# Kernel optimization log

Measured on AMD Instinct MI355X. Metric: run time of the kernel, lower is better.

The kernel has to match this reference:

```python
import jax, jax.numpy as jnp
import numpy as np

NUM_HEADS = 16
HEAD_DIM = 128  # hidden_size=2048 // num_heads=16


def setup_inputs() -> dict:
    key = jax.random.key(0)
    k1, k2, k3, k4, k5 = jax.random.split(key, 5)
    B, S, H = 4, 4096, 2048
    scale_in = 1.0 / np.sqrt(H)
    return {
        "x": jax.random.normal(k1, (B, S, H), dtype=jnp.float32),
        "Wqkv": jax.random.normal(k2, (H, 3 * H), dtype=jnp.float32) * scale_in,
        "bqkv": jax.random.normal(k3, (3 * H,), dtype=jnp.float32) * 0.01,
        "Wproj": jax.random.normal(k4, (H, H), dtype=jnp.float32) * scale_in,
        "bproj": jax.random.normal(k5, (H,), dtype=jnp.float32) * 0.01,
    }


def reference(x, Wqkv, bqkv, Wproj, bproj):
    B, S, hidden = x.shape
    H, D = NUM_HEADS, HEAD_DIM
    qkv = x @ Wqkv + bqkv                       # (B, S, 3*hidden)
    qkv = qkv.reshape(B, S, 3, H, D)
    q, k, v = qkv[:, :, 0], qkv[:, :, 1], qkv[:, :, 2]  # each (B, S, H, D)
    # Faithful to source: matmul over last two dims -> scores are (B, S, H, H)
    # (head-to-head attention per position; the repo never moved heads to dim 1).
    scores = jnp.einsum("bshd,bstd->bsht", q, k) / jnp.sqrt(jnp.asarray(D, x.dtype))
    weights = jax.nn.softmax(scores, axis=-1)    # (B, S, H, H)
    context = jnp.einsum("bsht,bstd->bshd", weights, v)  # (B, S, H, D)
    # Faithful reproduction of context.transpose(1, 2).contiguous().view(B, S, hidden)
    context = context.transpose(0, 2, 1, 3).reshape(B, S, hidden)
    return context @ Wproj + bproj
```

## Files before the change

kernel.cpp:

```cpp
#include <hip/hip_runtime.h>

typedef unsigned short u16;
typedef __attribute__((ext_vector_type(8))) short short8;
typedef __attribute__((ext_vector_type(4))) float float4v;

__device__ __forceinline__ u16 f2b(float f) {
  union { float f; unsigned u; } v; v.f = f;
  unsigned r = v.u + 0x7fffu + ((v.u >> 16) & 1u);
  return (u16)(r >> 16);
}

#define AS1(p) ((const __attribute__((address_space(1))) void*)(p))
#define AS3(p) ((__attribute__((address_space(3))) void*)(p))
#define MFMA16(a, b, c) __builtin_amdgcn_mfma_f32_16x16x32_bf16(a, b, c, 0, 0, 0)

__global__ __launch_bounds__(256) void cvt_bf16_kernel(const float* __restrict__ in,
                                                       u16* __restrict__ out, long n) {
  long i = ((long)blockIdx.x * 256 + threadIdx.x) * 8;
  if (i + 8 > n) return;
  float4v a = *(const float4v*)(in + i);
  float4v b = *(const float4v*)(in + i + 4);
  short8 o;
  o[0] = (short)f2b(a[0]); o[1] = (short)f2b(a[1]);
  o[2] = (short)f2b(a[2]); o[3] = (short)f2b(a[3]);
  o[4] = (short)f2b(b[0]); o[5] = (short)f2b(b[1]);
  o[6] = (short)f2b(b[2]); o[7] = (short)f2b(b[3]);
  *(short8*)(out + i) = o;
}

__global__ __launch_bounds__(256) void transpose_cvt_kernel(const float* __restrict__ in,
                                                            u16* __restrict__ out,
                                                            int rows, int cols) {
  __shared__ float tile[32][33];
  int bx = blockIdx.x * 32;
  int by = blockIdx.y * 32;
  int tx = threadIdx.x & 31, ty = threadIdx.x >> 5;
  for (int r = ty; r < 32; r += 8)
    tile[r][tx] = in[(long)(by + r) * cols + bx + tx];
  __syncthreads();
  for (int r = ty; r < 32; r += 8)
    out[(long)(bx + r) * rows + by + tx] = f2b(tile[tx][r]);
}

__global__ __launch_bounds__(512, 2) void gemm256_bt_bias(const u16* __restrict__ A,
                                                          const u16* __restrict__ B,
                                                          const float* __restrict__ bias,
                                                          void* __restrict__ Cout,
                                                          int M, int N, int K, int out_bf16) {
  __shared__ __align__(16) u16 As[2][2][8192];
  __shared__ __align__(16) u16 Bs[2][2][8192];

  const int t = threadIdx.x;
  const int lane = t & 63;
  const int w = t >> 6;
  const int wm = w >> 2;
  const int wn = w & 3;
  const int lm = lane & 15;
  const int lq = lane >> 4;

  const int nwg = gridDim.x * gridDim.y;
  const int orig = blockIdx.y * gridDim.x + blockIdx.x;
  const int qq = nwg >> 3, rr = nwg & 7;
  const int xcd = orig & 7, loc = orig >> 3;
  const int wgid = (xcd < rr ? xcd * (qq + 1) : rr * (qq + 1) + (xcd - rr) * qq) + loc;
  const int bx = wgid % gridDim.x;
  const int by = wgid / gridDim.x;

  const long row0 = (long)by * 256;
  const long col0 = (long)bx * 256;

  const int phys0 = t * 8;
  const int log0 = phys0 ^ (((phys0 >> 6) & 7) << 3);
  const long r0s = log0 >> 6; const int c0s = log0 & 63;
  const long r1s = r0s + 64;  const int c1s = c0s;

  const u16* Ag0 = A + (row0 + r0s) * K + c0s;
  const u16* Ag1 = A + (row0 + r1s) * K + c1s;
  const u16* Bg0 = B + (col0 + r0s) * K + c0s;
  const u16* Bg1 = B + (col0 + r1s) * K + c1s;
  const long hstride = 128L * (long)K;

  const int sb  = lm * 64 + ((lq * 8) ^ ((lm & 7) << 3));
  const int sbx = sb ^ 32;

  float4v acc[8][4] = {};
  const int NT = K >> 6;

  auto stA = [&](int buf, int h, int kt) {
    u16* d = &As[buf][h][0] + t * 8;
    const long ko = (long)kt * 64 + (long)h * hstride;
    __builtin_amdgcn_global_load_lds(AS1(Ag0 + ko), AS3(d), 16, 0, 0);
    __builtin_amdgcn_global_load_lds(AS1(Ag1 + ko), AS3(d + 4096), 16, 0, 0);
  };
  auto stB = [&](int buf, int h, int kt) {
    u16* d = &Bs[buf][h][0] + t * 8;
    const long ko = (long)kt * 64 + (long)h * hstride;
    __builtin_amdgcn_global_load_lds(AS1(Bg0 + ko), AS3(d), 16, 0, 0);
    __builtin_amdgcn_global_load_lds(AS1(Bg1 + ko), AS3(d + 4096), 16, 0, 0);
  };

  auto ktile = [&](int buf, int u) {
    asm volatile("" ::: "memory");
    const u16* Abl = &As[buf][wm][0] + sb;
    const u16* Abh = &As[buf][wm][0] + sbx;
    const u16* Bbl = &Bs[buf][wn >> 1][0] + (wn & 1) * 4096 + sb;
    const u16* Bbh = &Bs[buf][wn >> 1][0] + (wn & 1) * 4096 + sbx;
    const int kn  = (u + 1 < NT) ? u + 1 : NT - 1;
    const int kb2 = (u + 2 < NT) ? u + 2 : NT - 1;

    short8 bfr[4][2];
#pragma unroll
    for (int n = 0; n < 4; n++) {
      bfr[n][0] = *(const short8*)(Bbl + n * 1024);
      bfr[n][1] = *(const short8*)(Bbh + n * 1024);
    }
    {
      short8 a00 = *(const short8*)(Abl + 0);
      short8 a01 = *(const short8*)(Abh + 0);
      short8 a10 = *(const short8*)(Abl + 1024);
      short8 a11 = *(const short8*)(Abh + 1024);
      stA(buf ^ 1, 0, kn);
      asm volatile("s_waitcnt lgkmcnt(8)" ::: "memory");
      __builtin_amdgcn_s_barrier();
      asm volatile("s_waitcnt lgkmcnt(0)" ::: "memory");
      __builtin_amdgcn_s_setprio(1);
#pragma unroll
      for (int n = 0; n < 4; n++) {
        acc[0][n] = MFMA16(a00, bfr[n][0], acc[0][n]);
        acc[0][n] = MFMA16(a01, bfr[n][1], acc[0][n]);
        acc[1][n] = MFMA16(a10, bfr[n][0], acc[1][n]);
        acc[1][n] = MFMA16(a11, bfr[n][1], acc[1][n]);
      }
      __builtin_amdgcn_s_setprio(0);
      __builtin_amdgcn_s_barrier();
    }
#pragma unroll
    for (int p = 1; p < 4; p++) {
      short8 a00 = *(const short8*)(Abl + (2 * p) * 1024);
      short8 a01 = *(const short8*)(Abh + (2 * p) * 1024);
      short8 a10 = *(const short8*)(Abl + (2 * p + 1) * 1024);
      short8 a11 = *(const short8*)(Abh + (2 * p + 1) * 1024);
      if (p == 1)      stA(buf ^ 1, 1, kn);
      else if (p == 2) stB(buf, 0, kb2);
      else             stB(buf, 1, kb2);
      __builtin_amdgcn_s_barrier();
      asm volatile("s_waitcnt lgkmcnt(0)" ::: "memory");
      __builtin_amdgcn_s_setprio(1);
#pragma unroll
      for (int n = 0; n < 4; n++) {
        acc[2 * p][n]     = MFMA16(a00, bfr[n][0], acc[2 * p][n]);
        acc[2 * p][n]     = MFMA16(a01, bfr[n][1], acc[2 * p][n]);
        acc[2 * p + 1][n] = MFMA16(a10, bfr[n][0], acc[2 * p + 1][n]);
        acc[2 * p + 1][n] = MFMA16(a11, bfr[n][1], acc[2 * p + 1][n]);
      }
      __builtin_amdgcn_s_setprio(0);
      if (p == 3) asm volatile("s_waitcnt vmcnt(4)" ::: "memory");
      __builtin_amdgcn_s_barrier();
    }
  };

  stA(0, 0, 0); stA(0, 1, 0); stB(0, 0, 0); stB(0, 1, 0);
  const int k1 = (NT > 1) ? 1 : 0;
  stB(1, 0, k1); stB(1, 1, k1);
  asm volatile("s_waitcnt vmcnt(4)" ::: "memory");
  __builtin_amdgcn_s_barrier();

  for (int u = 0; u < NT; u += 2) {
    ktile(0, u);
    ktile(1, u + 1);
  }

#pragma unroll
  for (int n = 0; n < 4; n++) {
    const long cg = col0 + wn * 64 + n * 16 + lm;
    const float bv = bias[cg];
#pragma unroll
    for (int m = 0; m < 8; m++) {
      const long rbase = row0 + wm * 128 + m * 16 + lq * 4;
#pragma unroll
      for (int r = 0; r < 4; r++) {
        const float v = acc[m][n][r] + bv;
        const long idx = (rbase + r) * N + cg;
        if (out_bf16) ((u16*)Cout)[idx] = f2b(v);
        else          ((float*)Cout)[idx] = v;
      }
    }
  }
}

__global__ __launch_bounds__(256) void head_attn_kernel(const u16* __restrict__ qkv,
                                                        u16* __restrict__ ctx) {
  __shared__ __align__(16) u16 vt_s[4][128 * 16];
  __shared__ __align__(16) u16 ws_s[4][16 * 32];
  const int tid = threadIdx.x;
  const int lane = tid & 63;
  const int w = tid >> 6;
  const int lm = lane & 15, lq = lane >> 4;
  const int pos = blockIdx.x * 4 + w;
  const int b = pos >> 12, s = pos & 4095;
  const long rowb = (long)pos * 6144;

  u16* vt = vt_s[w];
  u16* wsp = ws_s[w];

  for (int i = lane; i < 16 * 32; i += 64) wsp[i] = 0;

  {
    int tt = lane >> 2, db = (lane & 3) * 32;
#pragma unroll
    for (int c = 0; c < 4; c++) {
      short8 vv = *(const short8*)(qkv + rowb + 4096 + tt * 128 + db + c * 8);
#pragma unroll
      for (int j = 0; j < 8; j++)
        vt[(db + c * 8 + j) * 16 + tt] = (u16)vv[j];
    }
  }
  __syncthreads();

  float4v st = {0.f, 0.f, 0.f, 0.f};
#pragma unroll
  for (int ks = 0; ks < 4; ks++) {
    short8 qa = *(const short8*)(qkv + rowb + lm * 128 + ks * 32 + lq * 8);
    short8 kb = *(const short8*)(qkv + rowb + 2048 + lm * 128 + ks * 32 + lq * 8);
    st = __builtin_amdgcn_mfma_f32_16x16x32_bf16(qa, kb, st, 0, 0, 0);
  }

  const float sc = 0.08838834764831845f * 1.4426950408889634f;
#pragma unroll
  for (int r = 0; r < 4; r++) {
    float z = st[r] * sc;
    float m = z;
    m = fmaxf(m, __shfl_xor(m, 1));
    m = fmaxf(m, __shfl_xor(m, 2));
    m = fmaxf(m, __shfl_xor(m, 4));
    m = fmaxf(m, __shfl_xor(m, 8));
    float p = exp2f(z - m);
    float ss = p;
    ss += __shfl_xor(ss, 1);
    ss += __shfl_xor(ss, 2);
    ss += __shfl_xor(ss, 4);
    ss += __shfl_xor(ss, 8);
    wsp[(lq * 4 + r) * 32 + lm] = f2b(p / ss);
  }
  __syncthreads();

  short8 wa = *(const short8*)(wsp + lm * 32 + lq * 8);
#pragma unroll
  for (int dt = 0; dt < 8; dt++) {
    short8 vb = *(const short8*)(vt + (dt * 16 + lm) * 16 + (lq & 1) * 8);
    float4v o = {0.f, 0.f, 0.f, 0.f};
    o = __builtin_amdgcn_mfma_f32_16x16x32_bf16(wa, vb, o, 0, 0, 0);
#pragma unroll
    for (int r = 0; r < 4; r++) {
      int h = lq * 4 + r;
      ctx[(((long)(b * 16 + h) * 4096 + s) * 128) + dt * 16 + lm] = f2b(o[r]);
    }
  }
}

extern "C" void kernel_launch(void* const* d_in, const int* in_sizes, int n_in,
                              void* d_out, int out_size, void* d_ws, size_t ws_size,
                              hipStream_t stream) {
  const float* x     = (const float*)d_in[0];
  const float* Wqkv  = (const float*)d_in[1];
  const float* bqkv  = (const float*)d_in[2];
  const float* Wproj = (const float*)d_in[3];
  const float* bproj = (const float*)d_in[4];
  float* out = (float*)d_out;

  u16* xb     = (u16*)d_ws;
  u16* WqkvT  = xb + 33554432L;
  u16* WprojT = WqkvT + 12582912L;
  u16* qkvb   = WprojT + 4194304L;
  u16* ctxb   = qkvb + 100663296L;

  cvt_bf16_kernel<<<33554432L / 2048, 256, 0, stream>>>(x, xb, 33554432L);
  transpose_cvt_kernel<<<dim3(6144 / 32, 2048 / 32), 256, 0, stream>>>(Wqkv, WqkvT, 2048, 6144);
  transpose_cvt_kernel<<<dim3(2048 / 32, 2048 / 32), 256, 0, stream>>>(Wproj, WprojT, 2048, 2048);

  gemm256_bt_bias<<<dim3(6144 / 256, 16384 / 256), 512, 0, stream>>>(
      xb, WqkvT, bqkv, qkvb, 16384, 6144, 2048, 1);

  head_attn_kernel<<<4096, 256, 0, stream>>>(qkvb, ctxb);

  gemm256_bt_bias<<<dim3(2048 / 256, 16384 / 256), 512, 0, stream>>>(
      ctxb, WprojT, bproj, out, 16384, 2048, 2048, 0);
}
```

Measured before the change: 900.2 us.

## Software-pipeline LDS fragment reads with MFMA and cut per-tile barriers

Restructures the GEMM K-loop so A fragments are double-buffered in registers (even/odd sets). Each phase's LDS reads are issued before the previous phase's MFMAs, and the next tile's first fragments and B fragments are prefetched before the tile boundary. Barriers per K-tile drop from eight to two, with waitcnts consolidated. This should hide LDS latency behind MFMA work, at the cost of more registers and more delicate ordering between the async global->LDS loads and the reads of shared buffers.

```diff
diff --git a/kernel.cpp b/kernel.cpp
--- a/kernel.cpp
+++ b/kernel.cpp
@@ -99,76 +99,104 @@
     __builtin_amdgcn_global_load_lds(AS1(Bg1 + ko), AS3(d + 4096), 16, 0, 0);
   };
 
-  auto ktile = [&](int buf, int u) {
-    asm volatile("" ::: "memory");
-    const u16* Abl = &As[buf][wm][0] + sb;
-    const u16* Abh = &As[buf][wm][0] + sbx;
-    const u16* Bbl = &Bs[buf][wn >> 1][0] + (wn & 1) * 4096 + sb;
-    const u16* Bbh = &Bs[buf][wn >> 1][0] + (wn & 1) * 4096 + sbx;
-    const int kn  = (u + 1 < NT) ? u + 1 : NT - 1;
-    const int kb2 = (u + 2 < NT) ? u + 2 : NT - 1;
-
-    short8 bfr[4][2];
-#pragma unroll
-    for (int n = 0; n < 4; n++) {
-      bfr[n][0] = *(const short8*)(Bbl + n * 1024);
-      bfr[n][1] = *(const short8*)(Bbh + n * 1024);
-    }
-    {
-      short8 a00 = *(const short8*)(Abl + 0);
-      short8 a01 = *(const short8*)(Abh + 0);
-      short8 a10 = *(const short8*)(Abl + 1024);
-      short8 a11 = *(const short8*)(Abh + 1024);
-      stA(buf ^ 1, 0, kn);
-      asm volatile("s_waitcnt lgkmcnt(8)" ::: "memory");
-      __builtin_amdgcn_s_barrier();
-      asm volatile("s_waitcnt lgkmcnt(0)" ::: "memory");
-      __builtin_amdgcn_s_setprio(1);
-#pragma unroll
-      for (int n = 0; n < 4; n++) {
-        acc[0][n] = MFMA16(a00, bfr[n][0], acc[0][n]);
-        acc[0][n] = MFMA16(a01, bfr[n][1], acc[0][n]);
-        acc[1][n] = MFMA16(a10, bfr[n][0], acc[1][n]);
-        acc[1][n] = MFMA16(a11, bfr[n][1], acc[1][n]);
-      }
-      __builtin_amdgcn_s_setprio(0);
-      __builtin_amdgcn_s_barrier();
-    }
-#pragma unroll
-    for (int p = 1; p < 4; p++) {
-      short8 a00 = *(const short8*)(Abl + (2 * p) * 1024);
-      short8 a01 = *(const short8*)(Abh + (2 * p) * 1024);
-      short8 a10 = *(const short8*)(Abl + (2 * p + 1) * 1024);
-      short8 a11 = *(const short8*)(Abh + (2 * p + 1) * 1024);
-      if (p == 1)      stA(buf ^ 1, 1, kn);
-      else if (p == 2) stB(buf, 0, kb2);
-      else             stB(buf, 1, kb2);
-      __builtin_amdgcn_s_barrier();
-      asm volatile("s_waitcnt lgkmcnt(0)" ::: "memory");
-      __builtin_amdgcn_s_setprio(1);
-#pragma unroll
-      for (int n = 0; n < 4; n++) {
-        acc[2 * p][n]     = MFMA16(a00, bfr[n][0], acc[2 * p][n]);
-        acc[2 * p][n]     = MFMA16(a01, bfr[n][1], acc[2 * p][n]);
-        acc[2 * p + 1][n] = MFMA16(a10, bfr[n][0], acc[2 * p + 1][n]);
-        acc[2 * p + 1][n] = MFMA16(a11, bfr[n][1], acc[2 * p + 1][n]);
-      }
-      __builtin_amdgcn_s_setprio(0);
-      if (p == 3) asm volatile("s_waitcnt vmcnt(4)" ::: "memory");
-      __builtin_amdgcn_s_barrier();
-    }
-  };
+  short8 bfr[4][2];
+  short8 aE[4];
+  short8 aO[4];
+
+#define MM(MP, F)                                                     \
+  do {                                                                \
+    __builtin_amdgcn_s_setprio(1);                                    \
+    _Pragma("unroll")                                                 \
+    for (int n = 0; n < 4; n++) {                                     \
+      acc[2 * (MP)][n]     = MFMA16((F)[0], bfr[n][0], acc[2 * (MP)][n]);     \
+      acc[2 * (MP)][n]     = MFMA16((F)[1], bfr[n][1], acc[2 * (MP)][n]);     \
+      acc[2 * (MP) + 1][n] = MFMA16((F)[2], bfr[n][0], acc[2 * (MP) + 1][n]); \
+      acc[2 * (MP) + 1][n] = MFMA16((F)[3], bfr[n][1], acc[2 * (MP) + 1][n]); \
+    }                                                                 \
+    __builtin_amdgcn_s_setprio(0);                                    \
+  } while (0)
 
   stA(0, 0, 0); stA(0, 1, 0); stB(0, 0, 0); stB(0, 1, 0);
   const int k1 = (NT > 1) ? 1 : 0;
   stB(1, 0, k1); stB(1, 1, k1);
   asm volatile("s_waitcnt vmcnt(4)" ::: "memory");
   __builtin_amdgcn_s_barrier();
-
-  for (int u = 0; u < NT; u += 2) {
-    ktile(0, u);
-    ktile(1, u + 1);
-  }
+  asm volatile("" ::: "memory");
+
+  {
+    const u16* Abl = &As[0][wm][0] + sb;
+    const u16* Abh = &As[0][wm][0] + sbx;
+    const u16* Bbl = &Bs[0][wn >> 1][0] + (wn & 1) * 4096 + sb;
+    const u16* Bbh = &Bs[0][wn >> 1][0] + (wn & 1) * 4096 + sbx;
+    aE[0] = *(const short8*)(Abl + 0);
+    aE[1] = *(const short8*)(Abh + 0);
+    aE[2] = *(const short8*)(Abl + 1024);
+    aE[3] = *(const short8*)(Abh + 1024);
+#pragma unroll
+    for (int n = 0; n < 4; n++) {
+      bfr[n][0] = *(const short8*)(Bbl + n * 1024);
+      bfr[n][1] = *(const short8*)(Bbh + n * 1024);
+    }
+  }
+
+  for (int u = 0; u < NT; u++) {
+    const int buf = u & 1;
+    const u16* Abl = &As[buf][wm][0] + sb;
+    const u16* Abh = &As[buf][wm][0] + sbx;
+    const int kn  = (u + 1 < NT) ? u + 1 : NT - 1;
+    const int kb2 = (u + 2 < NT) ? u + 2 : NT - 1;
+
+    stA(buf ^ 1, 0, kn);
+    aO[0] = *(const short8*)(Abl + 2 * 1024);
+    aO[1] = *(const short8*)(Abh + 2 * 1024);
+    aO[2] = *(const short8*)(Abl + 3 * 1024);
+    aO[3] = *(const short8*)(Abh + 3 * 1024);
+    MM(0, aE);
+
+    stA(buf ^ 1, 1, kn);
+    asm volatile("" ::: "memory");
+    __builtin_amdgcn_s_barrier();
+    asm volatile("" ::: "memory");
+    aE[0] = *(const short8*)(Abl + 4 * 1024);
+    aE[1] = *(const short8*)(Abh + 4 * 1024);
+    aE[2] = *(const short8*)(Abl + 5 * 1024);
+    aE[3] = *(const short8*)(Abh + 5 * 1024);
+    MM(1, aO);
+
+    stB(buf, 0, kb2);
+    aO[0] = *(const short8*)(Abl + 6 * 1024);
+    aO[1] = *(const short8*)(Abh + 6 * 1024);
+    aO[2] = *(const short8*)(Abl + 7 * 1024);
+    aO[3] = *(const short8*)(Abh + 7 * 1024);
+    MM(2, aE);
+
+    stB(buf, 1, kb2);
+    asm volatile("s_waitcnt lgkmcnt(0)" ::: "memory");
+    asm volatile("s_waitcnt vmcnt(4)" ::: "memory");
+    __builtin_amdgcn_s_barrier();
+    asm volatile("" ::: "memory");
+    if (u + 1 < NT) {
+      const int nb = buf ^ 1;
+      const u16* Anl = &As[nb][wm][0] + sb;
+      const u16* Anh = &As[nb][wm][0] + sbx;
+      const u16* Bnl = &Bs[nb][wn >> 1][0] + (wn & 1) * 4096 + sb;
+      const u16* Bnh = &Bs[nb][wn >> 1][0] + (wn & 1) * 4096 + sbx;
+      aE[0] = *(const short8*)(Anl + 0);
+      aE[1] = *(const short8*)(Anh + 0);
+      aE[2] = *(const short8*)(Anl + 1024);
+      aE[3] = *(const short8*)(Anh + 1024);
+      MM(3, aO);
+      asm volatile("" ::: "memory");
+#pragma unroll
+      for (int n = 0; n < 4; n++) {
+        bfr[n][0] = *(const short8*)(Bnl + n * 1024);
+        bfr[n][1] = *(const short8*)(Bnh + n * 1024);
+      }
+    } else {
+      MM(3, aO);
+    }
+  }
+#undef MM
 
 #pragma unroll
   for (int n = 0; n < 4; n++) {
```

After: 990.0 us. +10.0%, slower.
